# Kernel tuning notes

Measured on AMD Instinct MI355X. Metric: run time of the kernel, lower is better.

Reference implementation:

```python
import jax, jax.numpy as jnp
import numpy as np

B, H, W, C = 4, 64, 64, 256
CK = C // 8  # f/g projection dim = 32


def setup_inputs() -> dict:
    key = jax.random.key(0)
    ks = jax.random.split(key, 4)
    x = jax.random.normal(ks[0], (B, H, W, C), dtype=jnp.float32)
    Wf = jax.random.normal(ks[1], (C, CK), dtype=jnp.float32) * (1.0 / np.sqrt(C))
    Wg = jax.random.normal(ks[2], (C, CK), dtype=jnp.float32) * (1.0 / np.sqrt(C))
    Wh = jax.random.normal(ks[3], (C, C), dtype=jnp.float32) * (1.0 / np.sqrt(C))
    bf = jnp.zeros((CK,), jnp.float32)
    bg = jnp.zeros((CK,), jnp.float32)
    bh = jnp.zeros((C,), jnp.float32)
    return {"x": x, "Wf": Wf, "bf": bf, "Wg": Wg, "bg": bg, "Wh": Wh, "bh": bh}


def reference(x, Wf, bf, Wg, bg, Wh, bh):
    b, h, w, c = x.shape
    n = h * w
    xf = x.reshape(b, n, c)  # 1x1 conv == per-pixel matmul
    f = xf @ Wf + bf         # [b, n, c/8]  (keys)
    g = xf @ Wg + bg         # [b, n, c/8]  (queries)
    hh = xf @ Wh + bh        # [b, n, c]    (values)
    # s[i,j] = g_i . f_j  (tf.matmul(g, f, transpose_b=True))
    s = jnp.einsum('bik,bjk->bij', g, f)
    beta = jax.nn.softmax(s, axis=-1)
    o = jnp.einsum('bij,bjc->bic', beta, hh)
    return x + o.reshape(b, h, w, c)
```

## Files before the change

kernel.cpp:

```cpp
#include <hip/hip_runtime.h>
#include <math.h>

#define CDIM 256
#define CKD  32
#define NPIX 4096
#define BATCH 4
#define NMACRO (NPIX / 64)

typedef __attribute__((ext_vector_type(8)))  short bf16x8;
typedef __attribute__((ext_vector_type(16))) float f32x16;

#if __has_builtin(__builtin_amdgcn_exp2f)
#define EXP2(x) __builtin_amdgcn_exp2f(x)
#else
#define EXP2(x) exp2f(x)
#endif

__device__ inline ushort f2bf(float x) {
    unsigned u = __float_as_uint(x);
    u += 0x7fffu + ((u >> 16) & 1u);
    return (ushort)(u >> 16);
}
__device__ inline unsigned packbf(float a, float b) {
    return (unsigned)f2bf(a) | ((unsigned)f2bf(b) << 16);
}
__device__ inline unsigned cvtpk(float a, float b) {
    unsigned r;
    asm("v_cvt_pk_bf16_f32 %0, %1, %2" : "=v"(r) : "v"(a), "v"(b));
    return r;
}
__device__ inline void lane32swap(unsigned &a, unsigned &b) {
    asm("v_permlane32_swap_b32 %0, %1" : "+v"(a), "+v"(b));
}

#define LDS_ASYNC16(gptr, lptr) \
  __builtin_amdgcn_global_load_lds((const __attribute__((address_space(1))) void*)(gptr), \
                                   (__attribute__((address_space(3))) void*)(lptr), 16, 0, 0)

__global__ __launch_bounds__(256) void prep_kernel(
    const float* __restrict__ Wh, const float* __restrict__ Wf,
    const float* __restrict__ Wg, ushort* __restrict__ Wt)
{
    __shared__ float ls[64 * 65];
    const int tid = threadIdx.x;
    const int bid = blockIdx.x;

    if (bid < 16) {
        const int k0 = (bid & 3) * 64, c0 = (bid >> 2) * 64;
        #pragma unroll
        for (int i = 0; i < 16; ++i) {
            int r = i * 4 + (tid >> 6), c = tid & 63;
            ls[r * 65 + c] = Wh[(k0 + r) * 256 + c0 + c];
        }
        __syncthreads();
        #pragma unroll
        for (int i = 0; i < 16; ++i) {
            int cr = i * 4 + (tid >> 6), k = tid & 63;
            Wt[(c0 + cr) * 256 + k0 + k] = f2bf(ls[k * 65 + cr]);
        }
    } else {
        const float* W = (bid == 16) ? Wf : Wg;
        const int rbase = 256 + (bid - 16) * 32;
        #pragma unroll
        for (int kh2 = 0; kh2 < 2; ++kh2) {
            __syncthreads();
            #pragma unroll
            for (int i = 0; i < 16; ++i) {
                int flat = i * 256 + tid;
                int k = flat >> 5, c = flat & 31;
                ls[c * 129 + k] = W[(kh2 * 128 + k) * 32 + c];
            }
            __syncthreads();
            #pragma unroll
            for (int i = 0; i < 16; ++i) {
                int flat = i * 256 + tid;
                int c = flat >> 7, k = flat & 127;
                Wt[(rbase + c) * 256 + kh2 * 128 + k] = f2bf(ls[c * 129 + k]);
            }
        }
    }
}

__global__ __launch_bounds__(256) void proj_kernel(
    const float*  __restrict__ x,
    const ushort* __restrict__ Wt,
    const float*  __restrict__ bfp, const float* __restrict__ bgp,
    const float*  __restrict__ bhp,
    ushort* __restrict__ fo,
    ushort* __restrict__ go,
    ushort* __restrict__ glo,
    ushort* __restrict__ ht)
{
    __shared__ ushort wls[2][1280 * 8];
    __shared__ ushort xls[2][128 * 8];

    const int tid  = threadIdx.x;
    const int w    = tid >> 6;
    const int lane = tid & 63;
    const int hl   = lane >> 5;
    const int ln   = lane & 31;
    const int bid  = blockIdx.x;
    const long long px0 = (long long)bid * 32;
    const int b    = (int)(px0 >> 12);
    const int n0   = (int)(px0 & (NPIX - 1));
    const int kt   = n0 >> 6;
    const int koff = n0 & 63;

    const int sx_px = tid >> 3, sx_j = tid & 7;
    const int sx_o = sx_j >> 1, sx_h = sx_j & 1;
    const int sx_slot = sx_o * 32 + ((sx_px + 2 * sx_o) & 31);

    #pragma unroll
    for (int i = 0; i < 5; ++i) {
        int s = i * 256 + tid;
        int n = s >> 2, o = ((s & 3) - (n >> 1)) & 3;
        LDS_ASYNC16(Wt + n * 256 + o * 8, &wls[0][s * 8]);
    }
    {
        float4 v = *(const float4*)(x + (px0 + sx_px) * CDIM + sx_j * 4);
        uint2 p; p.x = packbf(v.x, v.y); p.y = packbf(v.z, v.w);
        *(uint2*)&xls[0][sx_slot * 8 + sx_h * 4] = p;
    }

    f32x16 acc0={0,0,0,0,0,0,0,0,0,0,0,0,0,0,0,0};
    f32x16 acc1={0,0,0,0,0,0,0,0,0,0,0,0,0,0,0,0};
    f32x16 accfg={0,0,0,0,0,0,0,0,0,0,0,0,0,0,0,0};

    for (int sl = 0; sl < 8; ++sl) {
        const int cur = sl & 1;
        __syncthreads();
        if (sl + 1 < 8) {
            const int nxt = cur ^ 1;
            #pragma unroll
            for (int i = 0; i < 5; ++i) {
                int s = i * 256 + tid;
                int n = s >> 2, o = ((s & 3) - (n >> 1)) & 3;
                LDS_ASYNC16(Wt + n * 256 + (sl + 1) * 32 + o * 8, &wls[nxt][s * 8]);
            }
            float4 v = *(const float4*)(x + (px0 + sx_px) * CDIM + (sl + 1) * 32 + sx_j * 4);
            uint2 p; p.x = packbf(v.x, v.y); p.y = packbf(v.z, v.w);
            *(uint2*)&xls[nxt][sx_slot * 8 + sx_h * 4] = p;
        }

        #pragma unroll
        for (int st = 0; st < 2; ++st) {
            const int o = st * 2 + hl;
            #define LDW(n) (*(const bf16x8*)&wls[cur][((n) * 4 + (((o) + ((n) >> 1)) & 3)) * 8])
            bf16x8 xb  = *(const bf16x8*)&xls[cur][(o * 32 + ((ln + 2 * o) & 31)) * 8];
            bf16x8 wa0 = LDW(w * 64 + ln);
            bf16x8 wa1 = LDW(w * 64 + 32 + ln);
            acc0 = __builtin_amdgcn_mfma_f32_32x32x16_bf16(wa0, xb, acc0, 0, 0, 0);
            acc1 = __builtin_amdgcn_mfma_f32_32x32x16_bf16(wa1, xb, acc1, 0, 0, 0);
            if (w < 2) {
                bf16x8 wfg = LDW(256 + w * 32 + ln);
                accfg = __builtin_amdgcn_mfma_f32_32x32x16_bf16(xb, wfg, accfg, 0, 0, 0);
            }
            #undef LDW
        }
    }

    ushort* htt = ht + ((long long)(b * 64 + kt) * CDIM) * 64 + koff;
    #pragma unroll
    for (int r = 0; r < 16; ++r) {
        const int rowD = (r & 3) + 8 * (r >> 2) + 4 * hl;
        int c0 = w * 64 + rowD, c1 = c0 + 32;
        htt[(long long)c0 * 64 + ln] = f2bf(acc0[r] + bhp[c0]);
        htt[(long long)c1 * 64 + ln] = f2bf(acc1[r] + bhp[c1]);
    }
    if (w < 2) {
        const float bb = (w ? bgp : bfp)[ln];
        const float scl = w ? 1.44269504088896f : 1.0f;
        #pragma unroll
        for (int r = 0; r < 16; ++r) {
            const int rowD = (r & 3) + 8 * (r >> 2) + 4 * hl;
            float v = (accfg[r] + bb) * scl;
            ushort hi = f2bf(v);
            long long idx = (px0 + rowD) * CKD + ln;
            if (w == 0) {
                fo[idx] = hi;
            } else {
                go[idx] = hi;
                float hif = __uint_as_float(((unsigned)hi) << 16);
                glo[idx] = f2bf(v - hif);
            }
        }
    }
}

__global__ __launch_bounds__(256, 3) void attn_kernel(
    const float*  __restrict__ x,
    const ushort* __restrict__ fk,
    const ushort* __restrict__ gq,
    const ushort* __restrict__ glo,
    const ushort* __restrict__ hv,
    float* __restrict__ out,
    float* __restrict__ Opart,
    float* __restrict__ Lpart,
    int nks)
{
    __shared__ ushort hh_lds[2][1024 * 8];
    __shared__ ushort f_lds[2][256 * 8];
    __shared__ float  l_red[128];

    const int tid  = threadIdx.x;
    const int w    = tid >> 6;
    const int lane = tid & 63;
    const int hl   = lane >> 5;
    const int ln   = lane & 31;

    const int bid = blockIdx.x;
    const int chs = bid & 1;
    const int b   = (bid >> 1) & 3;
    const int qt  = (bid >> 3) & 31;
    const int ks  = bid >> 8;
    const int q0  = qt * 128;
    const int kt0 = (ks * NMACRO) / nks;
    const int kt1 = ((ks + 1) * NMACRO) / nks;
    const int nmac = kt1 - kt0;

    const long long bbase = (long long)b * NPIX;
    const ushort* fbase = fk + bbase * CKD;
    const ushort* htb   = hv + (long long)b * 64 * (CDIM * 64);

    const ushort* gp  = gq  + (bbase + q0 + w * 32 + ln) * CKD;
    const ushort* glp = glo + (bbase + q0 + w * 32 + ln) * CKD;
    const bf16x8 ga0 = *(const bf16x8*)(gp + hl * 8);
    const bf16x8 ga1 = *(const bf16x8*)(gp + 16 + hl * 8);
    const bf16x8 gl0 = *(const bf16x8*)(glp + hl * 8);
    const bf16x8 gl1 = *(const bf16x8*)(glp + 16 + hl * 8);

    {
        const long long tb = (long long)kt0 * (CDIM * 64);
        #pragma unroll
        for (int i = 0; i < 4; ++i) {
            int s = i * 256 + tid;
            int c = s >> 3, j = ((s & 7) - c) & 7;
            LDS_ASYNC16(htb + tb + (long long)(chs * 128 + c) * 64 + j * 8, &hh_lds[0][s * 8]);
        }
        LDS_ASYNC16(fbase + (long long)(kt0 * 64 + (tid & 63)) * CKD + (tid >> 6) * 8,
                    &f_lds[0][tid * 8]);
    }

    const f32x16 Zv = {0,0,0,0,0,0,0,0,0,0,0,0,0,0,0,0};
    f32x16 acc0={0,0,0,0,0,0,0,0,0,0,0,0,0,0,0,0};
    f32x16 acc1={0,0,0,0,0,0,0,0,0,0,0,0,0,0,0,0};
    f32x16 acc2={0,0,0,0,0,0,0,0,0,0,0,0,0,0,0,0};
    f32x16 acc3={0,0,0,0,0,0,0,0,0,0,0,0,0,0,0,0};
    float lsA = 0.f, lsB = 0.f;

    #pragma unroll 2
    for (int m = 0; m < nmac; ++m) {
        const int kt = kt0 + m;
        const int cur = m & 1;
        __syncthreads();

        if (m + 1 < nmac) {
            const int nxt = cur ^ 1;
            const long long tb = (long long)(kt + 1) * (CDIM * 64);
            #pragma unroll
            for (int i = 0; i < 4; ++i) {
                int s = i * 256 + tid;
                int c = s >> 3, j = ((s & 7) - c) & 7;
                LDS_ASYNC16(htb + tb + (long long)(chs * 128 + c) * 64 + j * 8,
                            &hh_lds[nxt][s * 8]);
            }
            LDS_ASYNC16(fbase + (long long)((kt + 1) * 64 + (tid & 63)) * CKD + (tid >> 6) * 8,
                        &f_lds[nxt][tid * 8]);
        }

        #pragma unroll
        for (int kh = 0; kh < 2; ++kh) {
            f32x16 S, T;
            {
                bf16x8 fb0 = *(const bf16x8*)&f_lds[cur][((hl)     * 64 + kh * 32 + ln) * 8];
                bf16x8 fb1 = *(const bf16x8*)&f_lds[cur][((2 + hl) * 64 + kh * 32 + ln) * 8];
                __builtin_amdgcn_s_setprio(1);
                S = __builtin_amdgcn_mfma_f32_32x32x16_bf16(fb0, ga0, Zv, 0, 0, 0);
                T = __builtin_amdgcn_mfma_f32_32x32x16_bf16(fb0, gl0, Zv, 0, 0, 0);
                S = __builtin_amdgcn_mfma_f32_32x32x16_bf16(fb1, ga1, S, 0, 0, 0);
                T = __builtin_amdgcn_mfma_f32_32x32x16_bf16(fb1, gl1, T, 0, 0, 0);
                __builtin_amdgcn_s_setprio(0);
            }

            float p[16];
            #pragma unroll
            for (int r = 0; r < 16; ++r) {
                p[r] = EXP2(S[r] + T[r]);
                if (r & 1) lsB += p[r]; else lsA += p[r];
            }
            unsigned U[8];
            #pragma unroll
            for (int m2 = 0; m2 < 8; ++m2) U[m2] = cvtpk(p[2*m2], p[2*m2+1]);

            #pragma unroll
            for (int ck = 0; ck < 2; ++ck) {
                unsigned a0 = U[4*ck + 0], a1 = U[4*ck + 1];
                unsigned a2 = U[4*ck + 2], a3 = U[4*ck + 3];
                lane32swap(a0, a2);
                lane32swap(a1, a3);
                union { unsigned i[4]; bf16x8 v; } pf;
                pf.i[0] = a0; pf.i[1] = a1; pf.i[2] = a2; pf.i[3] = a3;
                bf16x8 pa = pf.v;
                const int oct = kh * 4 + ck * 2 + hl;
                const int c0 = ln, c1 = 32 + ln, c2 = 64 + ln, c3 = 96 + ln;
                bf16x8 hb0 = *(const bf16x8*)&hh_lds[cur][(c0 * 8 + ((oct + c0) & 7)) * 8];
                bf16x8 hb1 = *(const bf16x8*)&hh_lds[cur][(c1 * 8 + ((oct + c1) & 7)) * 8];
                bf16x8 hb2 = *(const bf16x8*)&hh_lds[cur][(c2 * 8 + ((oct + c2) & 7)) * 8];
                bf16x8 hb3 = *(const bf16x8*)&hh_lds[cur][(c3 * 8 + ((oct + c3) & 7)) * 8];
                __builtin_amdgcn_s_setprio(1);
                acc0 = __builtin_amdgcn_mfma_f32_32x32x16_bf16(pa, hb0, acc0, 0, 0, 0);
                acc1 = __builtin_amdgcn_mfma_f32_32x32x16_bf16(pa, hb1, acc1, 0, 0, 0);
                acc2 = __builtin_amdgcn_mfma_f32_32x32x16_bf16(pa, hb2, acc2, 0, 0, 0);
                acc3 = __builtin_amdgcn_mfma_f32_32x32x16_bf16(pa, hb3, acc3, 0, 0, 0);
                __builtin_amdgcn_s_setprio(0);
            }
        }
    }

    float lsum = lsA + lsB;
    lsum += __shfl_xor(lsum, 32);
    if (hl == 0) l_red[w * 32 + ln] = lsum;
    __syncthreads();

    if (Opart) {
        const long long pb = ((long long)(ks * BATCH + b) * NPIX + q0);
        if (chs == 0 && hl == 0) Lpart[pb + w * 32 + ln] = lsum;
        #pragma unroll
        for (int r = 0; r < 16; ++r) {
            int rowD = (r & 3) + 8 * (r >> 2) + 4 * hl;
            int ql = w * 32 + rowD;
            long long rg = (pb + ql) * CDIM + chs * 128 + ln;
            Opart[rg]      = acc0[r];
            Opart[rg + 32] = acc1[r];
            Opart[rg + 64] = acc2[r];
            Opart[rg + 96] = acc3[r];
        }
    } else {
        #pragma unroll
        for (int r = 0; r < 16; ++r) {
            int rowD = (r & 3) + 8 * (r >> 2) + 4 * hl;
            int ql = w * 32 + rowD;
            float linv = 1.f / l_red[ql];
            long long rg = (bbase + q0 + ql) * CDIM + chs * 128 + ln;
            out[rg]      = x[rg]      + acc0[r] * linv;
            out[rg + 32] = x[rg + 32] + acc1[r] * linv;
            out[rg + 64] = x[rg + 64] + acc2[r] * linv;
            out[rg + 96] = x[rg + 96] + acc3[r] * linv;
        }
    }
}

__global__ __launch_bounds__(256) void combine_kernel(
    const float* __restrict__ x, const float* __restrict__ Op,
    const float* __restrict__ Lp, float* __restrict__ out, int nks)
{
    const int tid = threadIdx.x, w = tid >> 6, lane = tid & 63;
    const int row = blockIdx.x * 4 + w;
    const int b = row >> 12, q = row & (NPIX - 1);

    float l = 0.f;
    for (int ks = 0; ks < nks; ++ks)
        l += Lp[(ks * BATCH + b) * NPIX + q];
    const float linv = 1.f / l;

    float4 a = {0.f, 0.f, 0.f, 0.f};
    for (int ks = 0; ks < nks; ++ks) {
        const float4 v = *(const float4*)&Op[
            (((long long)(ks * BATCH + b) * NPIX + q)) * CDIM + lane * 4];
        a.x += v.x; a.y += v.y; a.z += v.z; a.w += v.w;
    }
    const long long g = ((long long)b * NPIX + q) * CDIM + lane * 4;
    const float4 xv = *(const float4*)&x[g];
    float4 o;
    o.x = xv.x + a.x * linv;
    o.y = xv.y + a.y * linv;
    o.z = xv.z + a.z * linv;
    o.w = xv.w + a.w * linv;
    *(float4*)&out[g] = o;
}

extern "C" void kernel_launch(void* const* d_in, const int* in_sizes, int n_in,
                              void* d_out, int out_size, void* d_ws, size_t ws_size,
                              hipStream_t stream) {
    const float* x  = (const float*)d_in[0];
    const float* Wf = (const float*)d_in[1];
    const float* bf = (const float*)d_in[2];
    const float* Wg = (const float*)d_in[3];
    const float* bg = (const float*)d_in[4];
    const float* Wh = (const float*)d_in[5];
    const float* bh = (const float*)d_in[6];
    float* out = (float*)d_out;

    ushort* fbf = (ushort*)d_ws;
    ushort* gbf = fbf + BATCH * NPIX * CKD;
    ushort* glo = gbf + BATCH * NPIX * CKD;
    ushort* ht  = glo + BATCH * NPIX * CKD;
    ushort* Wt  = ht + BATCH * NPIX * CDIM;
    char*   pb  = (char*)(Wt + 320 * 256);

    const int NKS = 3;
    const size_t base_used = (size_t)(pb - (char*)d_ws);
    const size_t oelems = (size_t)NKS * BATCH * NPIX * CDIM;
    const size_t lelems = (size_t)NKS * BATCH * NPIX;
    float* Opart = nullptr;
    float* Lpart = nullptr;
    int nks = 1;
    if (ws_size >= base_used + (oelems + lelems) * sizeof(float)) {
        nks = NKS;
        Opart = (float*)pb;
        Lpart = Opart + oelems;
    }

    prep_kernel<<<dim3(18), 256, 0, stream>>>(Wh, Wf, Wg, Wt);
    proj_kernel<<<dim3(512), 256, 0, stream>>>(x, Wt, bf, bg, bh, fbf, gbf, glo, ht);
    attn_kernel<<<dim3(256 * nks), 256, 0, stream>>>(x, fbf, gbf, glo, ht, out,
                                                     Opart, Lpart, nks);
    if (nks > 1)
        combine_kernel<<<dim3(BATCH * NPIX / 4), 256, 0, stream>>>(x, Opart, Lpart, out, nks);
}
```

Baseline: 159.7 us.

## Cover all 256 value channels per attention block instead of splitting channel halves

Each attention block now produces all 256 output channels, so the QK^T scores and exp are computed once per query tile instead of once per channel half. This doubles the value tile held in LDS and the number of accumulators per wave, and lowers the occupancy hint from 3 to 2 blocks per CU. The key-split count now tries 4 before 3 when the workspace allows, to keep the grid large enough. The tradeoff is higher register and LDS pressure, fewer resident waves, and larger partial buffers for the combine kernel.

```diff
diff --git a/kernel.cpp b/kernel.cpp
--- a/kernel.cpp
+++ b/kernel.cpp
@@ -187,7 +187,7 @@
     }
 }
 
-__global__ __launch_bounds__(256, 3) void attn_kernel(
+__global__ __launch_bounds__(256, 2) void attn_kernel(
     const float*  __restrict__ x,
     const ushort* __restrict__ fk,
     const ushort* __restrict__ gq,
@@ -198,7 +198,7 @@
     float* __restrict__ Lpart,
     int nks)
 {
-    __shared__ ushort hh_lds[2][1024 * 8];
+    __shared__ ushort hh_lds[2][2048 * 8];
     __shared__ ushort f_lds[2][256 * 8];
     __shared__ float  l_red[128];
 
@@ -209,10 +209,9 @@
     const int ln   = lane & 31;
 
     const int bid = blockIdx.x;
-    const int chs = bid & 1;
-    const int b   = (bid >> 1) & 3;
-    const int qt  = (bid >> 3) & 31;
-    const int ks  = bid >> 8;
+    const int qt  = bid & 31;
+    const int b   = (bid >> 5) & 3;
+    const int ks  = bid >> 7;
     const int q0  = qt * 128;
     const int kt0 = (ks * NMACRO) / nks;
     const int kt1 = ((ks + 1) * NMACRO) / nks;
@@ -232,10 +231,10 @@
     {
         const long long tb = (long long)kt0 * (CDIM * 64);
         #pragma unroll
-        for (int i = 0; i < 4; ++i) {
+        for (int i = 0; i < 8; ++i) {
             int s = i * 256 + tid;
             int c = s >> 3, j = ((s & 7) - c) & 7;
-            LDS_ASYNC16(htb + tb + (long long)(chs * 128 + c) * 64 + j * 8, &hh_lds[0][s * 8]);
+            LDS_ASYNC16(htb + tb + (long long)c * 64 + j * 8, &hh_lds[0][s * 8]);
         }
         LDS_ASYNC16(fbase + (long long)(kt0 * 64 + (tid & 63)) * CKD + (tid >> 6) * 8,
                     &f_lds[0][tid * 8]);
@@ -246,6 +245,10 @@
     f32x16 acc1={0,0,0,0,0,0,0,0,0,0,0,0,0,0,0,0};
     f32x16 acc2={0,0,0,0,0,0,0,0,0,0,0,0,0,0,0,0};
     f32x16 acc3={0,0,0,0,0,0,0,0,0,0,0,0,0,0,0,0};
+    f32x16 acc4={0,0,0,0,0,0,0,0,0,0,0,0,0,0,0,0};
+    f32x16 acc5={0,0,0,0,0,0,0,0,0,0,0,0,0,0,0,0};
+    f32x16 acc6={0,0,0,0,0,0,0,0,0,0,0,0,0,0,0,0};
+    f32x16 acc7={0,0,0,0,0,0,0,0,0,0,0,0,0,0,0,0};
     float lsA = 0.f, lsB = 0.f;
 
     #pragma unroll 2
@@ -258,11 +261,10 @@
             const int nxt = cur ^ 1;
             const long long tb = (long long)(kt + 1) * (CDIM * 64);
             #pragma unroll
-            for (int i = 0; i < 4; ++i) {
+            for (int i = 0; i < 8; ++i) {
                 int s = i * 256 + tid;
                 int c = s >> 3, j = ((s & 7) - c) & 7;
-                LDS_ASYNC16(htb + tb + (long long)(chs * 128 + c) * 64 + j * 8,
-                            &hh_lds[nxt][s * 8]);
+                LDS_ASYNC16(htb + tb + (long long)c * 64 + j * 8, &hh_lds[nxt][s * 8]);
             }
             LDS_ASYNC16(fbase + (long long)((kt + 1) * 64 + (tid & 63)) * CKD + (tid >> 6) * 8,
                         &f_lds[nxt][tid * 8]);
@@ -302,16 +304,25 @@
                 pf.i[0] = a0; pf.i[1] = a1; pf.i[2] = a2; pf.i[3] = a3;
                 bf16x8 pa = pf.v;
                 const int oct = kh * 4 + ck * 2 + hl;
-                const int c0 = ln, c1 = 32 + ln, c2 = 64 + ln, c3 = 96 + ln;
-                bf16x8 hb0 = *(const bf16x8*)&hh_lds[cur][(c0 * 8 + ((oct + c0) & 7)) * 8];
-                bf16x8 hb1 = *(const bf16x8*)&hh_lds[cur][(c1 * 8 + ((oct + c1) & 7)) * 8];
-                bf16x8 hb2 = *(const bf16x8*)&hh_lds[cur][(c2 * 8 + ((oct + c2) & 7)) * 8];
-                bf16x8 hb3 = *(const bf16x8*)&hh_lds[cur][(c3 * 8 + ((oct + c3) & 7)) * 8];
+                const int base0 = (ln * 8 + ((oct + ln) & 7)) * 8;
+                const ushort* hbp = &hh_lds[cur][base0];
+                bf16x8 hb0 = *(const bf16x8*)(hbp);
+                bf16x8 hb1 = *(const bf16x8*)(hbp + 1 * 2048);
+                bf16x8 hb2 = *(const bf16x8*)(hbp + 2 * 2048);
+                bf16x8 hb3 = *(const bf16x8*)(hbp + 3 * 2048);
+                bf16x8 hb4 = *(const bf16x8*)(hbp + 4 * 2048);
+                bf16x8 hb5 = *(const bf16x8*)(hbp + 5 * 2048);
+                bf16x8 hb6 = *(const bf16x8*)(hbp + 6 * 2048);
+                bf16x8 hb7 = *(const bf16x8*)(hbp + 7 * 2048);
                 __builtin_amdgcn_s_setprio(1);
                 acc0 = __builtin_amdgcn_mfma_f32_32x32x16_bf16(pa, hb0, acc0, 0, 0, 0);
                 acc1 = __builtin_amdgcn_mfma_f32_32x32x16_bf16(pa, hb1, acc1, 0, 0, 0);
                 acc2 = __builtin_amdgcn_mfma_f32_32x32x16_bf16(pa, hb2, acc2, 0, 0, 0);
                 acc3 = __builtin_amdgcn_mfma_f32_32x32x16_bf16(pa, hb3, acc3, 0, 0, 0);
+                acc4 = __builtin_amdgcn_mfma_f32_32x32x16_bf16(pa, hb4, acc4, 0, 0, 0);
+                acc5 = __builtin_amdgcn_mfma_f32_32x32x16_bf16(pa, hb5, acc5, 0, 0, 0);
+                acc6 = __builtin_amdgcn_mfma_f32_32x32x16_bf16(pa, hb6, acc6, 0, 0, 0);
+                acc7 = __builtin_amdgcn_mfma_f32_32x32x16_bf16(pa, hb7, acc7, 0, 0, 0);
                 __builtin_amdgcn_s_setprio(0);
             }
         }
@@ -324,16 +335,20 @@
 
     if (Opart) {
         const long long pb = ((long long)(ks * BATCH + b) * NPIX + q0);
-        if (chs == 0 && hl == 0) Lpart[pb + w * 32 + ln] = lsum;
+        if (hl == 0) Lpart[pb + w * 32 + ln] = lsum;
         #pragma unroll
         for (int r = 0; r < 16; ++r) {
             int rowD = (r & 3) + 8 * (r >> 2) + 4 * hl;
             int ql = w * 32 + rowD;
-            long long rg = (pb + ql) * CDIM + chs * 128 + ln;
-            Opart[rg]      = acc0[r];
-            Opart[rg + 32] = acc1[r];
-            Opart[rg + 64] = acc2[r];
-            Opart[rg + 96] = acc3[r];
+            long long rg = (pb + ql) * CDIM + ln;
+            Opart[rg]       = acc0[r];
+            Opart[rg +  32] = acc1[r];
+            Opart[rg +  64] = acc2[r];
+            Opart[rg +  96] = acc3[r];
+            Opart[rg + 128] = acc4[r];
+            Opart[rg + 160] = acc5[r];
+            Opart[rg + 192] = acc6[r];
+            Opart[rg + 224] = acc7[r];
         }
     } else {
         #pragma unroll
@@ -341,11 +356,15 @@
             int rowD = (r & 3) + 8 * (r >> 2) + 4 * hl;
             int ql = w * 32 + rowD;
             float linv = 1.f / l_red[ql];
-            long long rg = (bbase + q0 + ql) * CDIM + chs * 128 + ln;
-            out[rg]      = x[rg]      + acc0[r] * linv;
-            out[rg + 32] = x[rg + 32] + acc1[r] * linv;
-            out[rg + 64] = x[rg + 64] + acc2[r] * linv;
-            out[rg + 96] = x[rg + 96] + acc3[r] * linv;
+            long long rg = (bbase + q0 + ql) * CDIM + ln;
+            out[rg]       = x[rg]       + acc0[r] * linv;
+            out[rg +  32] = x[rg +  32] + acc1[r] * linv;
+            out[rg +  64] = x[rg +  64] + acc2[r] * linv;
+            out[rg +  96] = x[rg +  96] + acc3[r] * linv;
+            out[rg + 128] = x[rg + 128] + acc4[r] * linv;
+            out[rg + 160] = x[rg + 160] + acc5[r] * linv;
+            out[rg + 192] = x[rg + 192] + acc6[r] * linv;
+            out[rg + 224] = x[rg + 224] + acc7[r] * linv;
         }
     }
 }
@@ -398,22 +417,24 @@
     ushort* Wt  = ht + BATCH * NPIX * CDIM;
     char*   pb  = (char*)(Wt + 320 * 256);
 
-    const int NKS = 3;
     const size_t base_used = (size_t)(pb - (char*)d_ws);
-    const size_t oelems = (size_t)NKS * BATCH * NPIX * CDIM;
-    const size_t lelems = (size_t)NKS * BATCH * NPIX;
     float* Opart = nullptr;
     float* Lpart = nullptr;
     int nks = 1;
-    if (ws_size >= base_used + (oelems + lelems) * sizeof(float)) {
-        nks = NKS;
-        Opart = (float*)pb;
-        Lpart = Opart + oelems;
+    for (int cand = 4; cand >= 3; --cand) {
+        size_t oe = (size_t)cand * BATCH * NPIX * CDIM;
+        size_t le = (size_t)cand * BATCH * NPIX;
+        if (ws_size >= base_used + (oe + le) * sizeof(float)) {
+            nks = cand;
+            Opart = (float*)pb;
+            Lpart = Opart + oe;
+            break;
+        }
     }
 
     prep_kernel<<<dim3(18), 256, 0, stream>>>(Wh, Wf, Wg, Wt);
     proj_kernel<<<dim3(512), 256, 0, stream>>>(x, Wt, bf, bg, bh, fbf, gbf, glo, ht);
-    attn_kernel<<<dim3(256 * nks), 256, 0, stream>>>(x, fbf, gbf, glo, ht, out,
+    attn_kernel<<<dim3(128 * nks), 256, 0, stream>>>(x, fbf, gbf, glo, ht, out,
                                                      Opart, Lpart, nks);
     if (nks > 1)
         combine_kernel<<<dim3(BATCH * NPIX / 4), 256, 0, stream>>>(x, Opart, Lpart, out, nks);
```

After: 154.2 us. -3.4%, faster.
